# Optimization experiments

Hardware: AMD Instinct MI355X
Metric: run time of the kernel (lower is better)

Reference implementation:

```python
import jax, jax.numpy as jnp
import numpy as np

B, S, D = 2, 2048, 2048
H, KV, HD = 32, 8, 64
REP = H // KV


def rotate_half(t):
    t1, t2 = t[..., : t.shape[-1] // 2], t[..., t.shape[-1] // 2 :]
    return jnp.concatenate((-t2, t1), axis=-1)


def setup_inputs() -> dict:
    key = jax.random.key(0)
    kx, kq, kk, kv, ko = jax.random.split(key, 5)
    x = jax.random.normal(kx, (B, S, D), dtype=jnp.float32) * 0.02
    # RoPE tables: shape [S, HD//2]; forward concatenates [cos, cos] to reach HD
    inv_freq = 1.0 / (10000.0 ** (np.arange(0, HD, 2, dtype=np.float32) / HD))
    freqs = np.outer(np.arange(S, dtype=np.float32), inv_freq)
    cos = jnp.asarray(np.cos(freqs), dtype=jnp.float32)
    sin = jnp.asarray(np.sin(freqs), dtype=jnp.float32)
    # causal additive mask [1,1,S,S]
    causal = np.tril(np.ones((S, S), dtype=bool))
    mask = jnp.asarray(np.where(causal, 0.0, -1e9).astype(np.float32))[None, None]
    s = 0.02
    wq = jax.random.normal(kq, (H * HD, D), dtype=jnp.float32) * s
    wk = jax.random.normal(kk, (KV * HD, D), dtype=jnp.float32) * s
    wv = jax.random.normal(kv, (KV * HD, D), dtype=jnp.float32) * s
    wo = jax.random.normal(ko, (D, H * HD), dtype=jnp.float32) * s
    return {"x": x, "cos": cos, "sin": sin, "mask": mask,
            "wq": wq, "wk": wk, "wv": wv, "wo": wo}


def reference(x, cos, sin, mask, wq, wk, wv, wo):
    b, s, d = x.shape
    # QKV projections (Linear with bias=False: x @ W^T)
    q = jnp.einsum("bsd,ed->bse", x, wq).reshape(b, s, H, HD)
    k = jnp.einsum("bsd,ed->bse", x, wk).reshape(b, s, KV, HD)
    v = jnp.einsum("bsd,ed->bse", x, wv).reshape(b, s, KV, HD)
    # RoPE: cos/sin [S, HD//2] -> [1, S, 1, HD]
    cc = jnp.concatenate([cos[:s], cos[:s]], axis=-1)[None, :, None, :]
    ss = jnp.concatenate([sin[:s], sin[:s]], axis=-1)[None, :, None, :]
    q = q * cc + rotate_half(q) * ss
    k = k * cc + rotate_half(k) * ss
    # GQA: group q heads by kv head (implicit broadcast instead of repeat_kv)
    q = q.transpose(0, 2, 1, 3).reshape(b, KV, REP, s, HD)  # [B,KV,REP,S,HD]
    k = k.transpose(0, 2, 1, 3)                              # [B,KV,S,HD]
    v = v.transpose(0, 2, 1, 3)                              # [B,KV,S,HD]
    scores = jnp.einsum("bkrqd,bksd->bkrqs", q, k) / np.sqrt(HD)
    scores = scores + mask[:, :, None, :, :]  # broadcast over rep dim
    probs = jax.nn.softmax(scores.astype(jnp.float32), axis=-1).astype(q.dtype)
    out = jnp.einsum("bkrqs,bksd->bkrqd", probs, v)
    out = out.transpose(0, 3, 1, 2, 4).reshape(b, s, H * HD)  # [B,S,H*HD]
    return jnp.einsum("bse,de->bsd", out, wo)
```

## Files before the change

kernel.cpp:

```cpp
#include <hip/hip_runtime.h>
#include <stdint.h>

#define DEV __device__ __forceinline__

typedef __bf16 bf16;
typedef __bf16 bf16x8 __attribute__((ext_vector_type(8)));
typedef __bf16 bf16x4v __attribute__((ext_vector_type(4)));
typedef float f32x4 __attribute__((ext_vector_type(4)));
typedef float f32x16 __attribute__((ext_vector_type(16)));
typedef int int2v __attribute__((ext_vector_type(2)));

constexpr int Bb = 2, Ss = 2048, Dd = 2048, Hh = 32, KVh = 8, HDd = 64;
constexpr int Mm = Bb * Ss;
constexpr int EQ = Hh * HDd;
constexpr int EKV = KVh * HDd;
constexpr int Ee = EQ + 2 * EKV;

DEV void gload16(const void* g, void* l) {
  __builtin_amdgcn_global_load_lds((const __attribute__((address_space(1))) uint32_t*)g,
                                   (__attribute__((address_space(3))) uint32_t*)l, 16, 0, 0);
}

#if __has_builtin(__builtin_amdgcn_exp2f)
DEV float exp2_fast(float x) { return __builtin_amdgcn_exp2f(x); }
#else
DEV float exp2_fast(float x) {
  float r;
  asm("v_exp_f32 %0, %1\n\ts_nop 0" : "=v"(r) : "v"(x));
  return r;
}
#endif
DEV uint32_t cvtpk(float lo, float hi) {
  uint32_t w;
  asm("v_cvt_pk_bf16_f32 %0, %1, %2" : "=v"(w) : "v"(lo), "v"(hi));
  return w;
}
DEV int2v pswap(uint32_t a, uint32_t b) {
  return __builtin_amdgcn_permlane32_swap((int)a, (int)b, false, false);
}
DEV float fu(uint32_t u) { union { uint32_t u; float f; } c; c.u = u; return c.f; }
DEV uint32_t uf(float f) { union { float f; uint32_t u; } c; c.f = f; return c.u; }

__global__ void cvt_kernel(const float* __restrict__ x, const float* __restrict__ wq,
                           const float* __restrict__ wk, const float* __restrict__ wv,
                           const float* __restrict__ wo,
                           bf16* __restrict__ xb, bf16* __restrict__ wqkvb,
                           bf16* __restrict__ wob) {
  const long NX = (long)Mm * Dd;
  const long NQ = (long)EQ * Dd;
  const long NK = (long)EKV * Dd;
  const long NO = (long)Dd * EQ;
  const long total4 = (NX + NQ + 2 * NK + NO) / 4;
  for (long i = (long)blockIdx.x * blockDim.x + threadIdx.x; i < total4;
       i += (long)gridDim.x * blockDim.x) {
    long e = i * 4;
    const float* src; bf16* dst;
    if (e < NX)                { src = x + e;                       dst = xb + e; }
    else if (e < NX + NQ)      { long o = e - NX;                   src = wq + o; dst = wqkvb + o; }
    else if (e < NX + NQ + NK) { long o = e - NX - NQ;              src = wk + o; dst = wqkvb + NQ + o; }
    else if (e < NX + NQ + 2*NK){ long o = e - NX - NQ - NK;        src = wv + o; dst = wqkvb + NQ + NK + o; }
    else                       { long o = e - NX - NQ - 2*NK;       src = wo + o; dst = wob + o; }
    float4 v = *(const float4*)src;
    bf16x4v b;
    b.x = (bf16)v.x; b.y = (bf16)v.y; b.z = (bf16)v.z; b.w = (bf16)v.w;
    *(bf16x4v*)dst = b;
  }
}

__global__ __launch_bounds__(512, 4)
void gemm1_kernel(const bf16* __restrict__ A, const bf16* __restrict__ Bt,
                  bf16* __restrict__ Cb, int Mn, int Nn, int Kn) {
  __shared__ __align__(16) bf16 As[2][128 * 64];
  __shared__ __align__(16) bf16 Bs[2][192 * 64];
  const int tid = threadIdx.x, wid = tid >> 6, lane = tid & 63;
  const int g = lane >> 4, c = lane & 15;
  const int wm = wid >> 2, wn = wid & 3;

  const int xcd = (int)blockIdx.x & 7;
  const int idx = (int)blockIdx.x >> 3;
  const int bi = (xcd >> 1) * 8 + (idx >> 3);
  const int bj = (xcd & 1) * 8 + (idx & 7);
  const long arow0 = (long)bi * 128, brow0 = (long)bj * 192;

  const int srow = tid >> 3, schk = tid & 7;
  const int cs = schk ^ (srow & 7);

  f32x4 acc[4][3] = {};

#pragma unroll
  for (int q = 0; q < 2; ++q)
    gload16(A + (arow0 + q * 64 + srow) * Kn + cs * 8,
            (char*)&As[0][0] + q * 8192 + tid * 16);
#pragma unroll
  for (int q = 0; q < 3; ++q)
    gload16(Bt + (brow0 + q * 64 + srow) * Kn + cs * 8,
            (char*)&Bs[0][0] + q * 8192 + tid * 16);
  __syncthreads();

  const int NT = Kn >> 6;
  for (int kt = 0; kt < NT; ++kt) {
    const char* pa = (const char*)&As[kt & 1][0];
    const char* pb = (const char*)&Bs[kt & 1][0];
    char* na = (char*)&As[(kt + 1) & 1][0];
    char* nb = (char*)&Bs[(kt + 1) & 1][0];
    const bool more = (kt + 1 < NT);
    bf16x8 bfr[3][2];

#pragma unroll
    for (int p = 0; p < 2; ++p) {
      bf16x8 af[2][2];
#pragma unroll
      for (int i2 = 0; i2 < 2; ++i2)
#pragma unroll
        for (int ks = 0; ks < 2; ++ks) {
          int r = wm * 64 + (2 * p + i2) * 16 + c;
          af[i2][ks] = *(const bf16x8*)(pa + r * 128 + (((ks * 4 + g) ^ (r & 7)) << 4));
        }
      if (p == 0) {
#pragma unroll
        for (int j = 0; j < 3; ++j)
#pragma unroll
          for (int ks = 0; ks < 2; ++ks) {
            int r = wn * 48 + j * 16 + c;
            bfr[j][ks] = *(const bf16x8*)(pb + r * 128 + (((ks * 4 + g) ^ (r & 7)) << 4));
          }
      }
      if (more) {
        if (p == 0) {
          gload16(Bt + (brow0 + 0 * 64 + srow) * Kn + (kt + 1) * 64 + cs * 8,
                  nb + 0 * 8192 + tid * 16);
          gload16(Bt + (brow0 + 1 * 64 + srow) * Kn + (kt + 1) * 64 + cs * 8,
                  nb + 1 * 8192 + tid * 16);
          gload16(A + (arow0 + 0 * 64 + srow) * Kn + (kt + 1) * 64 + cs * 8,
                  na + 0 * 8192 + tid * 16);
        } else {
          gload16(Bt + (brow0 + 2 * 64 + srow) * Kn + (kt + 1) * 64 + cs * 8,
                  nb + 2 * 8192 + tid * 16);
          gload16(A + (arow0 + 1 * 64 + srow) * Kn + (kt + 1) * 64 + cs * 8,
                  na + 1 * 8192 + tid * 16);
        }
      }
      __builtin_amdgcn_s_barrier();
      asm volatile("s_waitcnt lgkmcnt(0)" ::: "memory");
      __builtin_amdgcn_s_setprio(1);
#pragma unroll
      for (int i2 = 0; i2 < 2; ++i2)
#pragma unroll
        for (int j = 0; j < 3; ++j)
#pragma unroll
          for (int ks = 0; ks < 2; ++ks)
            acc[2 * p + i2][j] =
                __builtin_amdgcn_mfma_f32_16x16x32_bf16(af[i2][ks], bfr[j][ks],
                                                        acc[2 * p + i2][j], 0, 0, 0);
      __builtin_amdgcn_s_setprio(0);
      if (p == 0) __builtin_amdgcn_s_barrier();
    }
    __syncthreads();
  }

#pragma unroll
  for (int i = 0; i < 4; ++i)
#pragma unroll
    for (int j = 0; j < 3; ++j)
#pragma unroll
      for (int r = 0; r < 4; ++r) {
        long row = arow0 + wm * 64 + i * 16 + 4 * g + r;
        long col = brow0 + wn * 48 + j * 16 + c;
        Cb[row * Nn + col] = (bf16)acc[i][j][r];
      }
}

__global__ __launch_bounds__(512, 4)
void gemm2_kernel(const bf16* __restrict__ A, const bf16* __restrict__ Bt,
                  float* __restrict__ Cf, int Mn, int Nn, int Kn) {
  __shared__ __align__(16) bf16 As[2][128 * 64];
  __shared__ __align__(16) bf16 Bs[2][128 * 64];
  const int tid = threadIdx.x, wid = tid >> 6, lane = tid & 63;
  const int g = lane >> 4, c = lane & 15;
  const int wm = wid >> 2, wn = wid & 3;

  const int xcd = (int)blockIdx.x & 7;
  const int idx = (int)blockIdx.x >> 3;
  const int bi = (xcd >> 1) * 8 + (idx >> 3);
  const int bj = (xcd & 1) * 8 + (idx & 7);
  const long arow0 = (long)bi * 128, brow0 = (long)bj * 128;

  const int srow = tid >> 3, schk = tid & 7;
  const int cs = schk ^ (srow & 7);

  f32x4 acc[4][2] = {};

#pragma unroll
  for (int q = 0; q < 2; ++q) {
    gload16(A + (arow0 + q * 64 + srow) * Kn + cs * 8,
            (char*)&As[0][0] + q * 8192 + tid * 16);
    gload16(Bt + (brow0 + q * 64 + srow) * Kn + cs * 8,
            (char*)&Bs[0][0] + q * 8192 + tid * 16);
  }
  __syncthreads();

  const int NT = Kn >> 6;
  for (int kt = 0; kt < NT; ++kt) {
    const char* pa = (const char*)&As[kt & 1][0];
    const char* pb = (const char*)&Bs[kt & 1][0];
    char* na = (char*)&As[(kt + 1) & 1][0];
    char* nb = (char*)&Bs[(kt + 1) & 1][0];
    const bool more = (kt + 1 < NT);
    bf16x8 bfr[2][2];

#pragma unroll
    for (int p = 0; p < 2; ++p) {
      bf16x8 af[2][2];
#pragma unroll
      for (int i2 = 0; i2 < 2; ++i2)
#pragma unroll
        for (int ks = 0; ks < 2; ++ks) {
          int r = wm * 64 + (2 * p + i2) * 16 + c;
          af[i2][ks] = *(const bf16x8*)(pa + r * 128 + (((ks * 4 + g) ^ (r & 7)) << 4));
        }
      if (p == 0) {
#pragma unroll
        for (int j = 0; j < 2; ++j)
#pragma unroll
          for (int ks = 0; ks < 2; ++ks) {
            int r = wn * 32 + j * 16 + c;
            bfr[j][ks] = *(const bf16x8*)(pb + r * 128 + (((ks * 4 + g) ^ (r & 7)) << 4));
          }
      }
      if (more) {
        gload16(Bt + (brow0 + p * 64 + srow) * Kn + (kt + 1) * 64 + cs * 8,
                nb + p * 8192 + tid * 16);
        gload16(A + (arow0 + p * 64 + srow) * Kn + (kt + 1) * 64 + cs * 8,
                na + p * 8192 + tid * 16);
      }
      __builtin_amdgcn_s_barrier();
      asm volatile("s_waitcnt lgkmcnt(0)" ::: "memory");
      __builtin_amdgcn_s_setprio(1);
#pragma unroll
      for (int i2 = 0; i2 < 2; ++i2)
#pragma unroll
        for (int j = 0; j < 2; ++j)
#pragma unroll
          for (int ks = 0; ks < 2; ++ks)
            acc[2 * p + i2][j] =
                __builtin_amdgcn_mfma_f32_16x16x32_bf16(af[i2][ks], bfr[j][ks],
                                                        acc[2 * p + i2][j], 0, 0, 0);
      __builtin_amdgcn_s_setprio(0);
      if (p == 0) __builtin_amdgcn_s_barrier();
    }
    __syncthreads();
  }

#pragma unroll
  for (int i = 0; i < 4; ++i)
#pragma unroll
    for (int j = 0; j < 2; ++j)
#pragma unroll
      for (int r = 0; r < 4; ++r) {
        long row = arow0 + wm * 64 + i * 16 + 4 * g + r;
        long col = brow0 + wn * 32 + j * 16 + c;
        Cf[row * Nn + col] = acc[i][j][r];
      }
}

__global__ void kv_prep_kernel(const bf16* __restrict__ qkv, const float* __restrict__ cosT,
                               const float* __restrict__ sinT, bf16* __restrict__ kout,
                               bf16* __restrict__ vtb) {
  if (blockIdx.x < 512) {
    __shared__ __align__(16) unsigned short tile[64][72];
    int blk = blockIdx.x;
    int st = blk & 31, kvh = (blk >> 5) & 7, b = blk >> 8;
    int s0 = st * 64;
    int t = threadIdx.x;
#pragma unroll
    for (int rep = 0; rep < 2; ++rep) {
      int idx = t + rep * 256;
      int r = idx >> 3, cb = idx & 7;
      const bf16* src = qkv + ((long)(b * Ss + s0 + r)) * Ee + EQ + EKV + kvh * 64 + cb * 8;
      *(uint4*)&tile[r][cb * 8] = *(const uint4*)src;
    }
    __syncthreads();
#pragma unroll
    for (int rep = 0; rep < 2; ++rep) {
      int idx = t + rep * 256;
      int dd = idx >> 3, scb = idx & 7;
      union { unsigned short u[8]; uint4 v; } pk;
#pragma unroll
      for (int j = 0; j < 8; ++j) pk.u[j] = tile[scb * 8 + j][dd];
      long dst = ((long)((b * KVh + kvh) * 64 + dd)) * Ss + s0 + scb * 8;
      *(uint4*)&vtb[dst] = pk.v;
    }
  } else {
    int tid = (int)(blockIdx.x - 512) * blockDim.x + threadIdx.x;
    int d = tid & 31;
    int h = (tid >> 5) & (KVh - 1);
    int m = tid >> 8;
    if (m >= Mm) return;
    int s = m & (Ss - 1), b = m >> 11;
    float lo = (float)qkv[(long)m * Ee + EQ + h * 64 + d];
    float hi = (float)qkv[(long)m * Ee + EQ + h * 64 + d + 32];
    float cs = cosT[s * 32 + d], sn = sinT[s * 32 + d];
    long base = (((long)(b * KVh + h)) * Ss + s) * 64;
    kout[base + d]      = (bf16)(lo * cs - hi * sn);
    kout[base + d + 32] = (bf16)(hi * cs + lo * sn);
  }
}

__global__ __launch_bounds__(512)
void attn_kernel(const bf16* __restrict__ qkv, const float* __restrict__ cosT,
                 const float* __restrict__ sinT, const bf16* __restrict__ k,
                 const bf16* __restrict__ vt, bf16* __restrict__ o) {
  __shared__ __align__(16) bf16 Kt[2][2][64 * 64];
  __shared__ __align__(16) bf16 Vt[2][2][64 * 64];
  constexpr float SCL = 0.18033688f;

  const int tid = threadIdx.x, qw = tid >> 6, lane = tid & 63;
  const int ql = lane & 31, hi = lane >> 5;
  const int g6 = (int)(blockIdx.x >> 6);
  const int qt = (g6 < 4) ? (7 - g6) : (g6 - 4);
  const int bh = blockIdx.x & 63;
  const int b = bh >> 5, h = bh & 31;
  const int kvh = h >> 2;
  const int q0 = qt * 256;
  const int qw_q0 = q0 + qw * 32;

  const bf16* kbase = k + ((long)(b * KVh + kvh)) * Ss * 64;
  const bf16* vbase = vt + ((long)(b * KVh + kvh)) * 64 * Ss;

  const int srow = tid >> 3, scb = tid & 7;
  const int scbs = scb ^ (srow & 7);
  const int sdst = tid * 16;

  bf16x8 qf[4];
  {
    const int s_row = q0 + qw * 32 + ql;
    const bf16* qrow = qkv + ((long)(b * Ss + s_row)) * Ee + h * 64 + 8 * hi;
    bf16x8 qraw[4];
#pragma unroll
    for (int ks = 0; ks < 4; ++ks) qraw[ks] = *(const bf16x8*)(qrow + 16 * ks);
    float cs8[2][8], sn8[2][8];
#pragma unroll
    for (int ks2 = 0; ks2 < 2; ++ks2) {
      const float* cp = cosT + s_row * 32 + 16 * ks2 + 8 * hi;
      const float* sp = sinT + s_row * 32 + 16 * ks2 + 8 * hi;
      *(float4*)&cs8[ks2][0] = *(const float4*)cp;
      *(float4*)&cs8[ks2][4] = *(const float4*)(cp + 4);
      *(float4*)&sn8[ks2][0] = *(const float4*)sp;
      *(float4*)&sn8[ks2][4] = *(const float4*)(sp + 4);
    }
#pragma unroll
    for (int ks2 = 0; ks2 < 2; ++ks2)
#pragma unroll
      for (int j = 0; j < 8; ++j) {
        float lo = (float)qraw[ks2][j], hv = (float)qraw[ks2 + 2][j];
        qf[ks2][j]     = (bf16)((lo * cs8[ks2][j] - hv * sn8[ks2][j]) * SCL);
        qf[ks2 + 2][j] = (bf16)((hv * cs8[ks2][j] + lo * sn8[ks2][j]) * SCL);
      }
  }

  bf16x8 bones;
#pragma unroll
  for (int j = 0; j < 8; ++j) bones[j] = (bf16)1.0f;

  gload16(kbase + (long)srow * 64 + scbs * 8, (char*)&Kt[0][0][0] + sdst);
  gload16(kbase + ((long)64 + srow) * 64 + scbs * 8, (char*)&Kt[0][1][0] + sdst);
  gload16(vbase + (long)srow * Ss + scbs * 8, (char*)&Vt[0][0][0] + sdst);
  gload16(vbase + (long)srow * Ss + 64 + scbs * 8, (char*)&Vt[0][1][0] + sdst);
  __syncthreads();

  f32x16 Oacc0 = {}, Oacc1 = {}, lacc = {};
  const int qa = qw_q0 + ql;
  const int nt = 4 * qt + 4;
  const int ntp = nt >> 1;
  const int tdiag = qw_q0 >> 6;

  int cur = 0;
  for (int pp = 0; pp < ntp; ++pp) {
    if (pp + 1 < ntp) {
      int nb = cur ^ 1;
      long t0 = (long)(2 * pp + 2) * 64;
      gload16(kbase + (t0 + srow) * 64 + scbs * 8, (char*)&Kt[nb][0][0] + sdst);
      gload16(kbase + (t0 + 64 + srow) * 64 + scbs * 8, (char*)&Kt[nb][1][0] + sdst);
      gload16(vbase + (long)srow * Ss + t0 + scbs * 8, (char*)&Vt[nb][0][0] + sdst);
      gload16(vbase + (long)srow * Ss + t0 + 64 + scbs * 8, (char*)&Vt[nb][1][0] + sdst);
    }

#pragma unroll
    for (int half = 0; half < 2; ++half) {
      const int t = 2 * pp + half;
      if (64 * t < qw_q0 + 32) {
        f32x16 s0 = {}, s1 = {};
        const char* kt = (const char*)&Kt[cur][half][0];
#pragma unroll
        for (int ks = 0; ks < 4; ++ks) {
          int chk = ((2 * ks + hi) ^ (ql & 7)) << 4;
          bf16x8 kf0 = *(const bf16x8*)(kt + ql * 128 + chk);
          bf16x8 kf1 = *(const bf16x8*)(kt + (32 + ql) * 128 + chk);
          s0 = __builtin_amdgcn_mfma_f32_32x32x16_bf16(kf0, qf[ks], s0, 0, 0, 0);
          s1 = __builtin_amdgcn_mfma_f32_32x32x16_bf16(kf1, qf[ks], s1, 0, 0, 0);
        }

        if (t == tdiag) {
#pragma unroll
          for (int r = 0; r < 16; ++r) {
            int kv0 = t * 64 + (r & 3) + 8 * (r >> 2) + 4 * hi;
            if (kv0 > qa)      s0[r] = -1e30f;
            if (kv0 + 32 > qa) s1[r] = -1e30f;
          }
        }

#pragma unroll
        for (int r = 0; r < 16; ++r) {
          s0[r] = exp2_fast(s0[r]);
          s1[r] = exp2_fast(s1[r]);
        }

        const char* vtb0 = (const char*)&Vt[cur][half][0];
#pragma unroll
        for (int ks = 0; ks < 4; ++ks) {
          uint32_t pk01, pk23, pk45, pk67;
          if (ks < 2) {
            const int rb = (ks & 1) * 8;
            pk01 = cvtpk(s0[rb + 0], s0[rb + 1]);
            pk23 = cvtpk(s0[rb + 2], s0[rb + 3]);
            pk45 = cvtpk(s0[rb + 4], s0[rb + 5]);
            pk67 = cvtpk(s0[rb + 6], s0[rb + 7]);
          } else {
            const int rb = (ks & 1) * 8;
            pk01 = cvtpk(s1[rb + 0], s1[rb + 1]);
            pk23 = cvtpk(s1[rb + 2], s1[rb + 3]);
            pk45 = cvtpk(s1[rb + 4], s1[rb + 5]);
            pk67 = cvtpk(s1[rb + 6], s1[rb + 7]);
          }
          int2v w02 = pswap(pk01, pk45);
          int2v w13 = pswap(pk23, pk67);
          union { uint32_t u[4]; bf16x8 v; } pa;
          pa.u[0] = (uint32_t)w02.x; pa.u[1] = (uint32_t)w13.x;
          pa.u[2] = (uint32_t)w02.y; pa.u[3] = (uint32_t)w13.y;

          int chk = ((2 * ks + hi) ^ (ql & 7)) << 4;
          bf16x8 vf0 = *(const bf16x8*)(vtb0 + ql * 128 + chk);
          bf16x8 vf1 = *(const bf16x8*)(vtb0 + (32 + ql) * 128 + chk);
          Oacc0 = __builtin_amdgcn_mfma_f32_32x32x16_bf16(pa.v, vf0, Oacc0, 0, 0, 0);
          Oacc1 = __builtin_amdgcn_mfma_f32_32x32x16_bf16(pa.v, vf1, Oacc1, 0, 0, 0);
          lacc  = __builtin_amdgcn_mfma_f32_32x32x16_bf16(pa.v, bones, lacc, 0, 0, 0);
        }
      }
    }

    __syncthreads();
    cur ^= 1;
  }

#pragma unroll
  for (int r = 0; r < 16; ++r) {
    int qrow = (r & 3) + 8 * (r >> 2) + 4 * hi;
    float li = 1.0f / lacc[r];
    long orow = (long)b * Ss + q0 + 32 * qw + qrow;
    o[orow * EQ + h * 64 + ql]      = (bf16)(Oacc0[r] * li);
    o[orow * EQ + h * 64 + 32 + ql] = (bf16)(Oacc1[r] * li);
  }
}

extern "C" void kernel_launch(void* const* d_in, const int* in_sizes, int n_in,
                              void* d_out, int out_size, void* d_ws, size_t ws_size,
                              hipStream_t stream) {
  const float* x    = (const float*)d_in[0];
  const float* cosT = (const float*)d_in[1];
  const float* sinT = (const float*)d_in[2];
  const float* wq   = (const float*)d_in[4];
  const float* wk   = (const float*)d_in[5];
  const float* wv   = (const float*)d_in[6];
  const float* wo   = (const float*)d_in[7];

  if (ws_size < 104857600u) return;

  char* ws = (char*)d_ws;
  bf16* xb    = (bf16*)(ws + 0);
  bf16* wqkvb = (bf16*)(ws + 16777216);
  bf16* wob   = (bf16*)(ws + 29360128);
  bf16* qkvb  = (bf16*)(ws + 37748736);
  bf16* kb    = (bf16*)(ws + 79691776);
  bf16* vtb   = (bf16*)(ws + 83886080);
  bf16* attnb = (bf16*)(ws + 88080384);
  float* outp = (float*)d_out;

  cvt_kernel<<<dim3(2048), dim3(256), 0, stream>>>(x, wq, wk, wv, wo, xb, wqkvb, wob);
  gemm1_kernel<<<dim3((Mm / 128) * (Ee / 192)), dim3(512), 0, stream>>>(
      xb, wqkvb, qkvb, Mm, Ee, Dd);
  kv_prep_kernel<<<dim3(512 + (Mm * KVh * 32) / 256), dim3(256), 0, stream>>>(
      qkvb, cosT, sinT, kb, vtb);
  attn_kernel<<<dim3(512), dim3(512), 0, stream>>>(qkvb, cosT, sinT, kb, vtb, attnb);
  gemm2_kernel<<<dim3((Mm / 128) * (EQ / 128)), dim3(512), 0, stream>>>(
      attnb, wob, outp, Mm, EQ, EQ);
}
```

Baseline: 159.8 us.

## Restructure GEMM mainloops into per-B-chunk phases with vmcnt-based waits

Both GEMM kernels now load all A fragments once per k-tile, then process the B tile in 64-row chunks. Each chunk loads its B fragment, issues the next tile's global-to-LDS loads for the slot just freed, and runs MFMAs. The full __syncthreads at the end of each k-tile is replaced by finer s_waitcnt vmcnt counts plus s_barrier, so prefetch overlaps compute more evenly. The warp-to-column mapping changes from contiguous wn*48 or wn*32 to an interleaved j*64+wn*16 layout, and the epilogue is updated to match. The hand-tuned vmcnt counts are a correctness risk if they do not line up with the outstanding loads.

```diff
diff --git a/kernel.cpp b/kernel.cpp
--- a/kernel.cpp
+++ b/kernel.cpp
@@ -104,58 +104,84 @@
     char* na = (char*)&As[(kt + 1) & 1][0];
     char* nb = (char*)&Bs[(kt + 1) & 1][0];
     const bool more = (kt + 1 < NT);
-    bf16x8 bfr[3][2];
-
-#pragma unroll
-    for (int p = 0; p < 2; ++p) {
-      bf16x8 af[2][2];
-#pragma unroll
-      for (int i2 = 0; i2 < 2; ++i2)
-#pragma unroll
-        for (int ks = 0; ks < 2; ++ks) {
-          int r = wm * 64 + (2 * p + i2) * 16 + c;
-          af[i2][ks] = *(const bf16x8*)(pa + r * 128 + (((ks * 4 + g) ^ (r & 7)) << 4));
-        }
-      if (p == 0) {
-#pragma unroll
-        for (int j = 0; j < 3; ++j)
-#pragma unroll
-          for (int ks = 0; ks < 2; ++ks) {
-            int r = wn * 48 + j * 16 + c;
-            bfr[j][ks] = *(const bf16x8*)(pb + r * 128 + (((ks * 4 + g) ^ (r & 7)) << 4));
-          }
+
+    bf16x8 af[4][2];
+#pragma unroll
+    for (int i2 = 0; i2 < 4; ++i2)
+#pragma unroll
+      for (int ks = 0; ks < 2; ++ks) {
+        int r = wm * 64 + i2 * 16 + c;
+        af[i2][ks] = *(const bf16x8*)(pa + r * 128 + (((ks * 4 + g) ^ (r & 7)) << 4));
       }
-      if (more) {
-        if (p == 0) {
-          gload16(Bt + (brow0 + 0 * 64 + srow) * Kn + (kt + 1) * 64 + cs * 8,
-                  nb + 0 * 8192 + tid * 16);
-          gload16(Bt + (brow0 + 1 * 64 + srow) * Kn + (kt + 1) * 64 + cs * 8,
-                  nb + 1 * 8192 + tid * 16);
-          gload16(A + (arow0 + 0 * 64 + srow) * Kn + (kt + 1) * 64 + cs * 8,
-                  na + 0 * 8192 + tid * 16);
-        } else {
-          gload16(Bt + (brow0 + 2 * 64 + srow) * Kn + (kt + 1) * 64 + cs * 8,
-                  nb + 2 * 8192 + tid * 16);
-          gload16(A + (arow0 + 1 * 64 + srow) * Kn + (kt + 1) * 64 + cs * 8,
-                  na + 1 * 8192 + tid * 16);
-        }
-      }
+    bf16x8 bfr[2];
+#pragma unroll
+    for (int ks = 0; ks < 2; ++ks) {
+      int r = 0 * 64 + wn * 16 + c;
+      bfr[ks] = *(const bf16x8*)(pb + r * 128 + (((ks * 4 + g) ^ (r & 7)) << 4));
+    }
+    if (more) {
+      gload16(A + (arow0 + 0 * 64 + srow) * Kn + (kt + 1) * 64 + cs * 8,
+              na + 0 * 8192 + tid * 16);
+      gload16(A + (arow0 + 1 * 64 + srow) * Kn + (kt + 1) * 64 + cs * 8,
+              na + 1 * 8192 + tid * 16);
+      gload16(Bt + (brow0 + 0 * 64 + srow) * Kn + (kt + 1) * 64 + cs * 8,
+              nb + 0 * 8192 + tid * 16);
+    }
+    asm volatile("s_waitcnt lgkmcnt(0)" ::: "memory");
+    __builtin_amdgcn_s_setprio(1);
+#pragma unroll
+    for (int i2 = 0; i2 < 4; ++i2)
+#pragma unroll
+      for (int ks = 0; ks < 2; ++ks)
+        acc[i2][0] = __builtin_amdgcn_mfma_f32_16x16x32_bf16(af[i2][ks], bfr[ks],
+                                                             acc[i2][0], 0, 0, 0);
+    __builtin_amdgcn_s_setprio(0);
+    if (more) asm volatile("s_waitcnt vmcnt(4)" ::: "memory");
+    else      asm volatile("s_waitcnt vmcnt(1)" ::: "memory");
+    __builtin_amdgcn_s_barrier();
+
+#pragma unroll
+    for (int ks = 0; ks < 2; ++ks) {
+      int r = 1 * 64 + wn * 16 + c;
+      bfr[ks] = *(const bf16x8*)(pb + r * 128 + (((ks * 4 + g) ^ (r & 7)) << 4));
+    }
+    if (more)
+      gload16(Bt + (brow0 + 1 * 64 + srow) * Kn + (kt + 1) * 64 + cs * 8,
+              nb + 1 * 8192 + tid * 16);
+    asm volatile("s_waitcnt lgkmcnt(0)" ::: "memory");
+    __builtin_amdgcn_s_setprio(1);
+#pragma unroll
+    for (int i2 = 0; i2 < 4; ++i2)
+#pragma unroll
+      for (int ks = 0; ks < 2; ++ks)
+        acc[i2][1] = __builtin_amdgcn_mfma_f32_16x16x32_bf16(af[i2][ks], bfr[ks],
+                                                             acc[i2][1], 0, 0, 0);
+    __builtin_amdgcn_s_setprio(0);
+    if (more) asm volatile("s_waitcnt vmcnt(4)" ::: "memory");
+    else      asm volatile("s_waitcnt vmcnt(0)" ::: "memory");
+    __builtin_amdgcn_s_barrier();
+
+#pragma unroll
+    for (int ks = 0; ks < 2; ++ks) {
+      int r = 2 * 64 + wn * 16 + c;
+      bfr[ks] = *(const bf16x8*)(pb + r * 128 + (((ks * 4 + g) ^ (r & 7)) << 4));
+    }
+    if (more)
+      gload16(Bt + (brow0 + 2 * 64 + srow) * Kn + (kt + 1) * 64 + cs * 8,
+              nb + 2 * 8192 + tid * 16);
+    asm volatile("s_waitcnt lgkmcnt(0)" ::: "memory");
+    __builtin_amdgcn_s_setprio(1);
+#pragma unroll
+    for (int i2 = 0; i2 < 4; ++i2)
+#pragma unroll
+      for (int ks = 0; ks < 2; ++ks)
+        acc[i2][2] = __builtin_amdgcn_mfma_f32_16x16x32_bf16(af[i2][ks], bfr[ks],
+                                                             acc[i2][2], 0, 0, 0);
+    __builtin_amdgcn_s_setprio(0);
+    if (more) {
+      asm volatile("s_waitcnt vmcnt(2)" ::: "memory");
       __builtin_amdgcn_s_barrier();
-      asm volatile("s_waitcnt lgkmcnt(0)" ::: "memory");
-      __builtin_amdgcn_s_setprio(1);
-#pragma unroll
-      for (int i2 = 0; i2 < 2; ++i2)
-#pragma unroll
-        for (int j = 0; j < 3; ++j)
-#pragma unroll
-          for (int ks = 0; ks < 2; ++ks)
-            acc[2 * p + i2][j] =
-                __builtin_amdgcn_mfma_f32_16x16x32_bf16(af[i2][ks], bfr[j][ks],
-                                                        acc[2 * p + i2][j], 0, 0, 0);
-      __builtin_amdgcn_s_setprio(0);
-      if (p == 0) __builtin_amdgcn_s_barrier();
-    }
-    __syncthreads();
+    }
   }
 
 #pragma unroll
@@ -165,7 +191,7 @@
 #pragma unroll
       for (int r = 0; r < 4; ++r) {
         long row = arow0 + wm * 64 + i * 16 + 4 * g + r;
-        long col = brow0 + wn * 48 + j * 16 + c;
+        long col = brow0 + j * 64 + wn * 16 + c;
         Cb[row * Nn + col] = (bf16)acc[i][j][r];
       }
 }
@@ -206,49 +232,64 @@
     char* na = (char*)&As[(kt + 1) & 1][0];
     char* nb = (char*)&Bs[(kt + 1) & 1][0];
     const bool more = (kt + 1 < NT);
-    bf16x8 bfr[2][2];
-
-#pragma unroll
-    for (int p = 0; p < 2; ++p) {
-      bf16x8 af[2][2];
-#pragma unroll
-      for (int i2 = 0; i2 < 2; ++i2)
-#pragma unroll
-        for (int ks = 0; ks < 2; ++ks) {
-          int r = wm * 64 + (2 * p + i2) * 16 + c;
-          af[i2][ks] = *(const bf16x8*)(pa + r * 128 + (((ks * 4 + g) ^ (r & 7)) << 4));
-        }
-      if (p == 0) {
-#pragma unroll
-        for (int j = 0; j < 2; ++j)
-#pragma unroll
-          for (int ks = 0; ks < 2; ++ks) {
-            int r = wn * 32 + j * 16 + c;
-            bfr[j][ks] = *(const bf16x8*)(pb + r * 128 + (((ks * 4 + g) ^ (r & 7)) << 4));
-          }
+
+    bf16x8 af[4][2];
+#pragma unroll
+    for (int i2 = 0; i2 < 4; ++i2)
+#pragma unroll
+      for (int ks = 0; ks < 2; ++ks) {
+        int r = wm * 64 + i2 * 16 + c;
+        af[i2][ks] = *(const bf16x8*)(pa + r * 128 + (((ks * 4 + g) ^ (r & 7)) << 4));
       }
-      if (more) {
-        gload16(Bt + (brow0 + p * 64 + srow) * Kn + (kt + 1) * 64 + cs * 8,
-                nb + p * 8192 + tid * 16);
-        gload16(A + (arow0 + p * 64 + srow) * Kn + (kt + 1) * 64 + cs * 8,
-                na + p * 8192 + tid * 16);
-      }
+    bf16x8 bfr[2];
+#pragma unroll
+    for (int ks = 0; ks < 2; ++ks) {
+      int r = 0 * 64 + wn * 16 + c;
+      bfr[ks] = *(const bf16x8*)(pb + r * 128 + (((ks * 4 + g) ^ (r & 7)) << 4));
+    }
+    if (more) {
+      gload16(A + (arow0 + 0 * 64 + srow) * Kn + (kt + 1) * 64 + cs * 8,
+              na + 0 * 8192 + tid * 16);
+      gload16(Bt + (brow0 + 0 * 64 + srow) * Kn + (kt + 1) * 64 + cs * 8,
+              nb + 0 * 8192 + tid * 16);
+    }
+    asm volatile("s_waitcnt lgkmcnt(0)" ::: "memory");
+    __builtin_amdgcn_s_setprio(1);
+#pragma unroll
+    for (int i2 = 0; i2 < 4; ++i2)
+#pragma unroll
+      for (int ks = 0; ks < 2; ++ks)
+        acc[i2][0] = __builtin_amdgcn_mfma_f32_16x16x32_bf16(af[i2][ks], bfr[ks],
+                                                             acc[i2][0], 0, 0, 0);
+    __builtin_amdgcn_s_setprio(0);
+    if (more) asm volatile("s_waitcnt vmcnt(2)" ::: "memory");
+    else      asm volatile("s_waitcnt vmcnt(0)" ::: "memory");
+    __builtin_amdgcn_s_barrier();
+
+#pragma unroll
+    for (int ks = 0; ks < 2; ++ks) {
+      int r = 1 * 64 + wn * 16 + c;
+      bfr[ks] = *(const bf16x8*)(pb + r * 128 + (((ks * 4 + g) ^ (r & 7)) << 4));
+    }
+    if (more) {
+      gload16(A + (arow0 + 1 * 64 + srow) * Kn + (kt + 1) * 64 + cs * 8,
+              na + 1 * 8192 + tid * 16);
+      gload16(Bt + (brow0 + 1 * 64 + srow) * Kn + (kt + 1) * 64 + cs * 8,
+              nb + 1 * 8192 + tid * 16);
+    }
+    asm volatile("s_waitcnt lgkmcnt(0)" ::: "memory");
+    __builtin_amdgcn_s_setprio(1);
+#pragma unroll
+    for (int i2 = 0; i2 < 4; ++i2)
+#pragma unroll
+      for (int ks = 0; ks < 2; ++ks)
+        acc[i2][1] = __builtin_amdgcn_mfma_f32_16x16x32_bf16(af[i2][ks], bfr[ks],
+                                                             acc[i2][1], 0, 0, 0);
+    __builtin_amdgcn_s_setprio(0);
+    if (more) {
+      asm volatile("s_waitcnt vmcnt(1)" ::: "memory");
       __builtin_amdgcn_s_barrier();
-      asm volatile("s_waitcnt lgkmcnt(0)" ::: "memory");
-      __builtin_amdgcn_s_setprio(1);
-#pragma unroll
-      for (int i2 = 0; i2 < 2; ++i2)
-#pragma unroll
-        for (int j = 0; j < 2; ++j)
-#pragma unroll
-          for (int ks = 0; ks < 2; ++ks)
-            acc[2 * p + i2][j] =
-                __builtin_amdgcn_mfma_f32_16x16x32_bf16(af[i2][ks], bfr[j][ks],
-                                                        acc[2 * p + i2][j], 0, 0, 0);
-      __builtin_amdgcn_s_setprio(0);
-      if (p == 0) __builtin_amdgcn_s_barrier();
-    }
-    __syncthreads();
+    }
   }
 
 #pragma unroll
@@ -258,7 +299,7 @@
 #pragma unroll
       for (int r = 0; r < 4; ++r) {
         long row = arow0 + wm * 64 + i * 16 + 4 * g + r;
-        long col = brow0 + wn * 32 + j * 16 + c;
+        long col = brow0 + j * 64 + wn * 16 + c;
         Cf[row * Nn + col] = acc[i][j][r];
       }
 }
```

Result: no change. 158.6 us (-0.7%).
